# Performance work log

Measured on AMD Instinct MI355X. Metric: run time of the kernel, lower is better.

The kernel has to match this reference:

```python
import jax, jax.numpy as jnp
import numpy as np

B, HRES, WRES, C, HEADS, WS, SS = 32, 64, 64, 256, 8, 8, 4
N = WS * WS
HID = 4 * C
EPS = 1e-5


def _rel_pos_index(ws):
    coords = np.stack(np.meshgrid(np.arange(ws), np.arange(ws), indexing='ij'))  # [2,ws,ws]
    cf = coords.reshape(2, -1)
    rel = (cf[:, :, None] - cf[:, None, :]).transpose(1, 2, 0)  # [N,N,2]
    rel[:, :, 0] += ws - 1
    rel[:, :, 1] += ws - 1
    rel[:, :, 0] *= 2 * ws - 1
    return rel.sum(-1).reshape(-1)  # [N*N]


def _attn_mask(H, W, ws, ss):
    img = np.zeros((H, W))
    cnt = 0
    for hs in (slice(0, -ws), slice(-ws, -ss), slice(-ss, None)):
        for wsl in (slice(0, -ws), slice(-ws, -ss), slice(-ss, None)):
            img[hs, wsl] = cnt
            cnt += 1
    mw = img.reshape(H // ws, ws, W // ws, ws).transpose(0, 2, 1, 3).reshape(-1, ws * ws)
    am = mw[:, None, :] - mw[:, :, None]  # [nW,N,N]
    return np.where(am != 0, -100.0, 0.0).astype(np.float32)


_RPI = jnp.asarray(_rel_pos_index(WS))
_MASK = jnp.asarray(_attn_mask(HRES, WRES, WS, SS))  # [nW,N,N]


def _ln(x, g, b):
    m = x.mean(-1, keepdims=True)
    v = ((x - m) ** 2).mean(-1, keepdims=True)
    return (x - m) / jnp.sqrt(v + EPS) * g + b


def setup_inputs() -> dict:
    key = jax.random.key(0)
    ks = jax.random.split(key, 16)
    s = 0.02
    return {
        'x': jax.random.normal(ks[0], (B, HRES * WRES, C), jnp.float32),
        'norm1_g': jnp.ones((C,), jnp.float32),
        'norm1_b': jnp.zeros((C,), jnp.float32),
        'qkv_w': jax.random.normal(ks[1], (3 * C, C), jnp.float32) * s,
        'qkv_b': jnp.zeros((3 * C,), jnp.float32),
        'rpb_table': jax.random.normal(ks[2], ((2 * WS - 1) ** 2, HEADS), jnp.float32) * s,
        'proj_w': jax.random.normal(ks[3], (C, C), jnp.float32) * s,
        'proj_b': jnp.zeros((C,), jnp.float32),
        'norm2_g': jnp.ones((C,), jnp.float32),
        'norm2_b': jnp.zeros((C,), jnp.float32),
        'fc1_w': jax.random.normal(ks[4], (HID, C), jnp.float32) * s,
        'fc1_b': jnp.zeros((HID,), jnp.float32),
        'fc2_w': jax.random.normal(ks[5], (C, HID), jnp.float32) * s,
        'fc2_b': jnp.zeros((C,), jnp.float32),
        'H': HRES,
        'W': WRES,
    }


def reference(x, norm1_g, norm1_b, qkv_w, qkv_b, rpb_table, proj_w, proj_b,
              norm2_g, norm2_b, fc1_w, fc1_b, fc2_w, fc2_b, H, W):
    Bn, L, Cd = x.shape
    ws, ss, nh = WS, SS, HEADS
    hd = Cd // nh
    shortcut = x
    h = _ln(x, norm1_g, norm1_b).reshape(Bn, H, W, Cd)
    # cyclic shift (H,W divisible by ws -> no padding needed)
    h = jnp.roll(h, (-ss, -ss), axis=(1, 2))
    # window partition: [B,H,W,C] -> [B*nW, N, C]
    h = h.reshape(Bn, H // ws, ws, W // ws, ws, Cd).transpose(0, 1, 3, 2, 4, 5).reshape(-1, N, Cd)
    qkv = (h @ qkv_w.T + qkv_b).reshape(-1, N, 3, nh, hd).transpose(2, 0, 3, 1, 4)
    q, k, v = qkv[0], qkv[1], qkv[2]  # [B_,h,N,d]
    attn = jnp.einsum('bhnd,bhmd->bhnm', q * (hd ** -0.5), k)
    rpb = rpb_table[_RPI].reshape(N, N, nh).transpose(2, 0, 1)  # [h,N,N]
    attn = attn + rpb[None]
    nW = _MASK.shape[0]
    attn = attn.reshape(Bn, nW, nh, N, N) + _MASK[None, :, None]
    attn = jax.nn.softmax(attn.reshape(-1, nh, N, N), axis=-1)
    o = jnp.einsum('bhnm,bhmd->bhnd', attn, v).transpose(0, 2, 1, 3).reshape(-1, N, Cd)
    o = o @ proj_w.T + proj_b
    # window reverse + reverse shift
    o = o.reshape(Bn, H // ws, W // ws, ws, ws, Cd).transpose(0, 1, 3, 2, 4, 5).reshape(Bn, H, W, Cd)
    o = jnp.roll(o, (ss, ss), axis=(1, 2)).reshape(Bn, L, Cd)
    x = shortcut + o
    h2 = _ln(x, norm2_g, norm2_b)
    h2 = jax.nn.gelu(h2 @ fc1_w.T + fc1_b, approximate=False)
    return x + (h2 @ fc2_w.T + fc2_b)
```

## Files before the change

### kernel.cpp

```cpp
#include <hip/hip_runtime.h>
#include <hip/hip_bf16.h>
#include <stdint.h>

typedef __bf16 bf16_t;
typedef __bf16 bf16x8 __attribute__((ext_vector_type(8)));
typedef __bf16 bf16x4 __attribute__((ext_vector_type(4)));
typedef float f32x4 __attribute__((ext_vector_type(4)));

#define MROWS 131072

__device__ __forceinline__ bf16_t to_bf16(float f) {
  __hip_bfloat16 h = __float2bfloat16(f);
  return *reinterpret_cast<bf16_t*>(&h);
}

__device__ __forceinline__ f32x4 mfma16(bf16x8 a, bf16x8 b, f32x4 c) {
  return __builtin_amdgcn_mfma_f32_16x16x32_bf16(a, b, c, 0, 0, 0);
}

__device__ __forceinline__ void gload16(const void* g, void* l) {
  __builtin_amdgcn_global_load_lds(
      (const __attribute__((address_space(1))) void*)g,
      (__attribute__((address_space(3))) void*)l, 16, 0, 0);
}

__device__ __forceinline__ int map_row(int m) {
  int b   = m >> 12;
  int rem = m & 4095;
  int win = rem >> 6;
  int n   = rem & 63;
  int gh  = ((win >> 3) << 3) + (n >> 3);
  int gw  = ((win & 7) << 3) + (n & 7);
  int sh  = (gh + 4) & 63;
  int sw  = (gw + 4) & 63;
  return (b << 12) + (sh << 6) + sw;
}

__global__ __launch_bounds__(256) void cvt_all(const float* __restrict__ qkv_w,
                                               const float* __restrict__ proj_w,
                                               const float* __restrict__ fc1_w,
                                               const float* __restrict__ fc2_w,
                                               bf16_t* __restrict__ qkv_o,
                                               bf16_t* __restrict__ proj_o,
                                               bf16_t* __restrict__ fc1_o,
                                               bf16_t* __restrict__ fc2_o) {
  int i = blockIdx.x * 256 + threadIdx.x;
  if (i < 196608)       qkv_o[i] = to_bf16(qkv_w[i]);
  else if (i < 262144)  proj_o[i - 196608] = to_bf16(proj_w[i - 196608]);
  else if (i < 524288)  fc1_o[i - 262144] = to_bf16(fc1_w[i - 262144]);
  else                  fc2_o[i - 524288] = to_bf16(fc2_w[i - 524288]);
}

__global__ __launch_bounds__(256) void bias_kernel(const float* __restrict__ rpbt,
                                                   float* __restrict__ bias) {
  int idx = blockIdx.x * 256 + threadIdx.x;
  int m = idx & 63, n = (idx >> 6) & 63, h = (idx >> 12) & 7, c = idx >> 15;
  int yn = n >> 3, xn = n & 7, ym = m >> 3, xm = m & 7;
  float v = rpbt[((yn - ym + 7) * 15 + (xn - xm + 7)) * 8 + h];
  int rn = (c & 2) ? (yn < 4 ? 1 : 2) : 0;
  int cn = (c & 1) ? (xn < 4 ? 1 : 2) : 0;
  int rm = (c & 2) ? (ym < 4 ? 1 : 2) : 0;
  int cm = (c & 1) ? (xm < 4 ? 1 : 2) : 0;
  if (rn * 3 + cn != rm * 3 + cm) v -= 100.0f;
  bias[idx] = v;
}

template <bool PERM>
__global__ __launch_bounds__(256) void ln_kernel(const float* __restrict__ xin,
                                                 const float* __restrict__ g,
                                                 const float* __restrict__ b,
                                                 bf16_t* __restrict__ out) {
  int row  = (blockIdx.x << 2) + (threadIdx.x >> 6);
  int lane = threadIdx.x & 63;
  int src  = PERM ? map_row(row) : row;
  float4 v = *reinterpret_cast<const float4*>(xin + (size_t)src * 256 + (lane << 2));
  float s = v.x + v.y + v.z + v.w;
#pragma unroll
  for (int d = 1; d < 64; d <<= 1) s += __shfl_xor(s, d);
  float mean = s * 0.00390625f;
  float ax = v.x - mean, ay = v.y - mean, az = v.z - mean, aw = v.w - mean;
  float s2 = ax * ax + ay * ay + az * az + aw * aw;
#pragma unroll
  for (int d = 1; d < 64; d <<= 1) s2 += __shfl_xor(s2, d);
  float rstd = rsqrtf(s2 * 0.00390625f + 1e-5f);
  float4 gv = *reinterpret_cast<const float4*>(g + (lane << 2));
  float4 bv = *reinterpret_cast<const float4*>(b + (lane << 2));
  bf16x4 o4;
  o4[0] = to_bf16(ax * rstd * gv.x + bv.x);
  o4[1] = to_bf16(ay * rstd * gv.y + bv.y);
  o4[2] = to_bf16(az * rstd * gv.z + bv.z);
  o4[3] = to_bf16(aw * rstd * gv.w + bv.w);
  *reinterpret_cast<bf16x4*>(out + (size_t)row * 256 + (lane << 2)) = o4;
}

template <int EPI>
__global__ __launch_bounds__(1024) void gemm256p(const bf16_t* __restrict__ A,
                                                 const bf16_t* __restrict__ W,
                                                 const float* __restrict__ bias,
                                                 void* __restrict__ outp,
                                                 void* __restrict__ outp2,
                                                 void* __restrict__ outp3,
                                                 const float* __restrict__ resid,
                                                 const float* __restrict__ n2g,
                                                 const float* __restrict__ n2b,
                                                 bf16_t* __restrict__ x2n,
                                                 int M, int N, int K, int NBN) {
  extern __shared__ __align__(16) char smem[];
  bf16_t* As  = (bf16_t*)smem;
  bf16_t* Bs  = As + 32768;
  float*  lnS = (float*)(Bs + 32768);
  float*  lnQ = lnS + 1024;
  float*  lnMR = lnQ + 1024;
  const int tid  = threadIdx.x;
  const int lane = tid & 63, lo = lane & 15, hi = lane >> 4;
  const int wid  = tid >> 6, wm = wid >> 2, wn = wid & 3;
  const int cpx = gridDim.x >> 3;
  const int wg  = (blockIdx.x & 7) * cpx + (blockIdx.x >> 3);
  const int bn = (wg % NBN) << 8, bm = (wg / NBN) << 8;
  f32x4 acc[4][4] = {};

#define STG(buf, kt)                                                        \
  {                                                                         \
    _Pragma("unroll") for (int l = 0; l < 2; ++l) {                         \
      int ch = (l << 10) + tid;                                             \
      int row = ch >> 3, sl = (ch & 7) ^ (row & 7);                         \
      gload16(A + (size_t)(bm + row) * K + ((kt) << 6) + (sl << 3),         \
              &As[((buf) << 14) + (ch << 3)]);                              \
      gload16(W + (size_t)(bn + row) * K + ((kt) << 6) + (sl << 3),         \
              &Bs[((buf) << 14) + (ch << 3)]);                              \
    }                                                                       \
  }

  const int nt = K >> 6;
  STG(0, 0);
  STG(1, 1);
  asm volatile("s_waitcnt vmcnt(4)" ::: "memory");
  __builtin_amdgcn_s_barrier();

  const int arow = (wm << 6) + lo;
  const int brow = (wn << 6) + lo;
  for (int t = 0; t < nt; ++t) {
    const int p = t & 1;
    const bf16_t* as = &As[p << 14];
    const bf16_t* bs = &Bs[p << 14];
    bf16x8 af0[4], bf0[4];
#pragma unroll
    for (int mf = 0; mf < 4; ++mf) {
      int r = arow + (mf << 4);
      af0[mf] = *reinterpret_cast<const bf16x8*>(&as[(r << 6) + ((hi ^ (r & 7)) << 3)]);
    }
#pragma unroll
    for (int nf = 0; nf < 4; ++nf) {
      int r = brow + (nf << 4);
      bf0[nf] = *reinterpret_cast<const bf16x8*>(&bs[(r << 6) + ((hi ^ (r & 7)) << 3)]);
    }
    __builtin_amdgcn_s_setprio(1);
#pragma unroll
    for (int mf = 0; mf < 4; ++mf)
#pragma unroll
      for (int nf = 0; nf < 4; ++nf)
        acc[mf][nf] = mfma16(af0[mf], bf0[nf], acc[mf][nf]);
    __builtin_amdgcn_s_setprio(0);
    bf16x8 af1[4], bf1[4];
#pragma unroll
    for (int mf = 0; mf < 4; ++mf) {
      int r = arow + (mf << 4);
      af1[mf] = *reinterpret_cast<const bf16x8*>(&as[(r << 6) + (((4 + hi) ^ (r & 7)) << 3)]);
    }
#pragma unroll
    for (int nf = 0; nf < 4; ++nf) {
      int r = brow + (nf << 4);
      bf1[nf] = *reinterpret_cast<const bf16x8*>(&bs[(r << 6) + (((4 + hi) ^ (r & 7)) << 3)]);
    }
    asm volatile("s_waitcnt lgkmcnt(0)" ::: "memory");
    __builtin_amdgcn_sched_barrier(0);
    __builtin_amdgcn_s_barrier();
    if (t + 2 < nt) STG(p, t + 2);
    __builtin_amdgcn_s_setprio(1);
#pragma unroll
    for (int mf = 0; mf < 4; ++mf)
#pragma unroll
      for (int nf = 0; nf < 4; ++nf)
        acc[mf][nf] = mfma16(af1[mf], bf1[nf], acc[mf][nf]);
    __builtin_amdgcn_s_setprio(0);
    if (t + 2 < nt)      { asm volatile("s_waitcnt vmcnt(4)" ::: "memory"); }
    else if (t + 1 < nt) { asm volatile("s_waitcnt vmcnt(0)" ::: "memory"); }
    __builtin_amdgcn_s_barrier();
  }
#undef STG

  float bv4[4];
#pragma unroll
  for (int nf = 0; nf < 4; ++nf) bv4[nf] = bias[bn + (wn << 6) + (nf << 4) + lo];

  if constexpr (EPI == 2) {
    float* o = (float*)outp;
    float gv[4], bnv[4];
#pragma unroll
    for (int nf = 0; nf < 4; ++nf) {
      int col = bn + (wn << 6) + (nf << 4) + lo;
      gv[nf] = n2g[col]; bnv[nf] = n2b[col];
    }
#pragma unroll
    for (int mf = 0; mf < 4; ++mf)
#pragma unroll
      for (int r = 0; r < 4; ++r) {
        int rl = (wm << 6) + (mf << 4) + (hi << 2) + r;
        int xr = map_row(bm + rl);
        float s = 0.f, q = 0.f;
#pragma unroll
        for (int nf = 0; nf < 4; ++nf) {
          int col = bn + (wn << 6) + (nf << 4) + lo;
          size_t idx = (size_t)xr * 256 + col;
          float v = resid[idx] + acc[mf][nf][r] + bv4[nf];
          acc[mf][nf][r] = v;
          o[idx] = v;
          s += v; q += v * v;
        }
#pragma unroll
        for (int d = 1; d < 16; d <<= 1) { s += __shfl_xor(s, d); q += __shfl_xor(q, d); }
        if (lo == 0) { lnS[(rl << 2) + wn] = s; lnQ[(rl << 2) + wn] = q; }
      }
    __syncthreads();
    if (tid < 256) {
      float s = lnS[tid << 2] + lnS[(tid << 2) + 1] + lnS[(tid << 2) + 2] + lnS[(tid << 2) + 3];
      float q = lnQ[tid << 2] + lnQ[(tid << 2) + 1] + lnQ[(tid << 2) + 2] + lnQ[(tid << 2) + 3];
      float mean = s * 0.00390625f;
      float var  = q * 0.00390625f - mean * mean;
      lnMR[tid << 1] = mean;
      lnMR[(tid << 1) + 1] = rsqrtf(var + 1e-5f);
    }
    __syncthreads();
#pragma unroll
    for (int mf = 0; mf < 4; ++mf)
#pragma unroll
      for (int r = 0; r < 4; ++r) {
        int rl = (wm << 6) + (mf << 4) + (hi << 2) + r;
        int xr = map_row(bm + rl);
        float mean = lnMR[rl << 1], rstd = lnMR[(rl << 1) + 1];
#pragma unroll
        for (int nf = 0; nf < 4; ++nf) {
          int col = bn + (wn << 6) + (nf << 4) + lo;
          x2n[(size_t)xr * 256 + col] = to_bf16((acc[mf][nf][r] - mean) * rstd * gv[nf] + bnv[nf]);
        }
      }
  } else {
#pragma unroll
    for (int mf = 0; mf < 4; ++mf)
#pragma unroll
      for (int r = 0; r < 4; ++r) {
        int row = bm + (wm << 6) + (mf << 4) + (hi << 2) + r;
        if constexpr (EPI == 3) {
          float* o = (float*)outp;
#pragma unroll
          for (int nf = 0; nf < 4; ++nf) {
            int col = bn + (wn << 6) + (nf << 4) + lo;
            size_t idx = (size_t)row * 256 + col;
            o[idx] = o[idx] + acc[mf][nf][r] + bv4[nf];
          }
        } else if constexpr (EPI == 4) {
#pragma unroll
          for (int nf = 0; nf < 4; ++nf) {
            int col = bn + (wn << 6) + (nf << 4) + lo;
            bf16_t* base = (col < 256) ? (bf16_t*)outp
                          : (col < 512) ? (bf16_t*)outp2 : (bf16_t*)outp3;
            int hd = (col >> 5) & 7, d = col & 31;
            base[((size_t)hd * MROWS + row) * 32 + d] = to_bf16(acc[mf][nf][r] + bv4[nf]);
          }
        } else {
          bf16_t* o = (bf16_t*)outp;
#pragma unroll
          for (int nf = 0; nf < 4; ++nf) {
            int col = bn + (wn << 6) + (nf << 4) + lo;
            float v = acc[mf][nf][r] + bv4[nf];
            if constexpr (EPI == 1) v = 0.5f * v * (1.0f + erff(v * 0.70710678118654752f));
            o[(size_t)row * N + col] = to_bf16(v);
          }
        }
      }
  }
}

template <int EPI>
__global__ __launch_bounds__(256) void gemm_bt(const bf16_t* __restrict__ A,
                                               const bf16_t* __restrict__ W,
                                               const float* __restrict__ bias,
                                               void* __restrict__ outp,
                                               int M, int N, int K, int NBN) {
  __shared__ __align__(16) bf16_t As[3 * 128 * 32];
  __shared__ __align__(16) bf16_t Bs[3 * 128 * 32];
  const int tid  = threadIdx.x;
  const int lane = tid & 63, lo = lane & 15, hi = lane >> 4;
  const int wave = tid >> 6;
  const int cpx = gridDim.x >> 3;
  const int wg  = (blockIdx.x & 7) * cpx + (blockIdx.x >> 3);
  const int bn = (wg % NBN) << 7, bm = (wg / NBN) << 7;
  const int wr = (wave >> 1) << 6, wc = (wave & 1) << 6;
  f32x4 acc[4][4] = {};

#define STAGE(buf, kt)                                                         \
  {                                                                            \
    int k0s = (kt) << 5;                                                       \
    _Pragma("unroll") for (int it = 0; it < 2; ++it) {                         \
      int ch = (it << 8) + tid;                                                \
      int r = ch >> 2;                                                         \
      int kf = ((ch & 3) ^ ((r >> 1) & 3)) << 3;                               \
      gload16(A + (size_t)(bm + r) * K + k0s + kf, &As[((buf) << 12) + (ch << 3)]); \
      gload16(W + (size_t)(bn + r) * K + k0s + kf, &Bs[((buf) << 12) + (ch << 3)]); \
    }                                                                          \
  }

  const int nt = K >> 5;
  STAGE(0, 0);
  STAGE(1, 1);

  int cb = 0;
  for (int t = 0; t < nt; ++t) {
    if (t + 1 < nt) { asm volatile("s_waitcnt vmcnt(4)" ::: "memory"); }
    else            { asm volatile("s_waitcnt vmcnt(0)" ::: "memory"); }
    __builtin_amdgcn_s_barrier();
    if (t + 2 < nt) {
      int sb = (cb == 0) ? 2 : cb - 1;
      STAGE(sb, t + 2);
    }
    const bf16_t* as = &As[cb << 12];
    const bf16_t* bs = &Bs[cb << 12];
    bf16x8 af[4], bfr[4];
#pragma unroll
    for (int i = 0; i < 4; ++i) {
      int ra = wr + (i << 4) + lo;
      af[i] = *reinterpret_cast<const bf16x8*>(&as[ra * 32 + ((hi ^ ((ra >> 1) & 3)) << 3)]);
    }
#pragma unroll
    for (int j = 0; j < 4; ++j) {
      int rb = wc + (j << 4) + lo;
      bfr[j] = *reinterpret_cast<const bf16x8*>(&bs[rb * 32 + ((hi ^ ((rb >> 1) & 3)) << 3)]);
    }
    __builtin_amdgcn_s_setprio(1);
#pragma unroll
    for (int i = 0; i < 4; ++i)
#pragma unroll
      for (int j = 0; j < 4; ++j)
        acc[i][j] = mfma16(af[i], bfr[j], acc[i][j]);
    __builtin_amdgcn_s_setprio(0);
    cb = (cb == 2) ? 0 : cb + 1;
  }
#undef STAGE

  float bv[4];
#pragma unroll
  for (int j = 0; j < 4; ++j) bv[j] = bias[bn + wc + (j << 4) + lo];

#pragma unroll
  for (int i = 0; i < 4; ++i)
#pragma unroll
    for (int r = 0; r < 4; ++r) {
      int row = bm + wr + (i << 4) + (hi << 2) + r;
      float* o = (float*)outp;
#pragma unroll
      for (int j = 0; j < 4; ++j) {
        int col = bn + wc + (j << 4) + lo;
        size_t idx = (size_t)row * 256 + col;
        o[idx] = o[idx] + acc[i][j][r] + bv[j];
      }
    }
}

__global__ __launch_bounds__(256) void attn_kernel(const bf16_t* __restrict__ qh,
                                                   const bf16_t* __restrict__ kh,
                                                   const bf16_t* __restrict__ vh,
                                                   const float* __restrict__ bias,
                                                   bf16_t* __restrict__ o) {
  __shared__ __align__(16) bf16_t Pl[4][64 * 72];
  __shared__ __align__(16) bf16_t Vt[4][32 * 72];
  const int wave = threadIdx.x >> 6, lane = threadIdx.x & 63;
  const int lo = lane & 15, hi = lane >> 4;
  const int id = (blockIdx.x << 2) + wave;
  const int win = id >> 3, h = id & 7;
  const size_t hb = ((size_t)h * MROWS + (size_t)win * 64) * 32;
  const bf16_t* qb = qh + hb;
  const bf16_t* kb = kh + hb;
  const bf16_t* vb = vh + hb;

  const bf16_t* vbl = vb + lane * 32;
#pragma unroll
  for (int c4 = 0; c4 < 4; ++c4) {
    bf16x8 v8 = *reinterpret_cast<const bf16x8*>(vbl + (c4 << 3));
#pragma unroll
    for (int e = 0; e < 8; ++e) Vt[wave][((c4 << 3) + e) * 72 + lane] = v8[e];
  }

  bf16x8 qa[4], ka[4];
#pragma unroll
  for (int i = 0; i < 4; ++i)
    qa[i] = *reinterpret_cast<const bf16x8*>(qb + ((i << 4) + lo) * 32 + (hi << 3));
#pragma unroll
  for (int j = 0; j < 4; ++j)
    ka[j] = *reinterpret_cast<const bf16x8*>(kb + ((j << 4) + lo) * 32 + (hi << 3));
  f32x4 s[4][4] = {};
#pragma unroll
  for (int i = 0; i < 4; ++i)
#pragma unroll
    for (int j = 0; j < 4; ++j) s[i][j] = mfma16(qa[i], ka[j], s[i][j]);

  const int wh = (win & 63) >> 3, ww = win & 7;
  const int cls = ((wh == 7) ? 2 : 0) + ((ww == 7) ? 1 : 0);
  const float* bb = bias + ((size_t)cls * 8 + h) * 4096;
  const float scale = 0.17677669529663687f;

  float pinv[4][4];
#pragma unroll
  for (int i = 0; i < 4; ++i) {
#pragma unroll
    for (int r = 0; r < 4; ++r) {
      int n = (i << 4) + (hi << 2) + r;
      const float* brow = bb + n * 64 + lo;
      float vals[4], mx = -1e30f;
#pragma unroll
      for (int j = 0; j < 4; ++j) {
        float val = s[i][j][r] * scale + brow[j << 4];
        vals[j] = val;
        mx = fmaxf(mx, val);
      }
#pragma unroll
      for (int d = 1; d < 16; d <<= 1) mx = fmaxf(mx, __shfl_xor(mx, d));
      float sum = 0.0f;
#pragma unroll
      for (int j = 0; j < 4; ++j) {
        float p = __expf(vals[j] - mx);
        sum += p;
        Pl[wave][n * 72 + (j << 4) + lo] = to_bf16(p);
      }
#pragma unroll
      for (int d = 1; d < 16; d <<= 1) sum += __shfl_xor(sum, d);
      pinv[i][r] = 1.0f / sum;
    }
  }

  __syncthreads();

  f32x4 oa[4][2] = {};
#pragma unroll
  for (int kt = 0; kt < 2; ++kt) {
    bf16x8 pa[4], va[2];
#pragma unroll
    for (int i = 0; i < 4; ++i)
      pa[i] = *reinterpret_cast<const bf16x8*>(&Pl[wave][((i << 4) + lo) * 72 + (kt << 5) + (hi << 3)]);
#pragma unroll
    for (int dt = 0; dt < 2; ++dt)
      va[dt] = *reinterpret_cast<const bf16x8*>(&Vt[wave][((dt << 4) + lo) * 72 + (kt << 5) + (hi << 3)]);
#pragma unroll
    for (int i = 0; i < 4; ++i)
#pragma unroll
      for (int dt = 0; dt < 2; ++dt) oa[i][dt] = mfma16(pa[i], va[dt], oa[i][dt]);
  }

  bf16_t* ob = o + (size_t)win * (64 * 256) + h * 32;
#pragma unroll
  for (int i = 0; i < 4; ++i)
#pragma unroll
    for (int r = 0; r < 4; ++r) {
      int n = (i << 4) + (hi << 2) + r;
      float piv = pinv[i][r];
#pragma unroll
      for (int dt = 0; dt < 2; ++dt)
        ob[(size_t)n * 256 + (dt << 4) + lo] = to_bf16(oa[i][dt][r] * piv);
    }
}

extern "C" void kernel_launch(void* const* d_in, const int* in_sizes, int n_in,
                              void* d_out, int out_size, void* d_ws, size_t ws_size,
                              hipStream_t stream) {
  const float* x      = (const float*)d_in[0];
  const float* n1g    = (const float*)d_in[1];
  const float* n1b    = (const float*)d_in[2];
  const float* qkv_w  = (const float*)d_in[3];
  const float* qkv_b  = (const float*)d_in[4];
  const float* rpbt   = (const float*)d_in[5];
  const float* proj_w = (const float*)d_in[6];
  const float* proj_b = (const float*)d_in[7];
  const float* n2g    = (const float*)d_in[8];
  const float* n2b    = (const float*)d_in[9];
  const float* fc1_w  = (const float*)d_in[10];
  const float* fc1_b  = (const float*)d_in[11];
  const float* fc2_w  = (const float*)d_in[12];
  const float* fc2_b  = (const float*)d_in[13];
  float* out = (float*)d_out;
  char*  ws  = (char*)d_ws;

  const size_t MB64 = 67108864;
  bf16_t* hln  = (bf16_t*)(ws);
  bf16_t* obuf = (bf16_t*)(ws);
  bf16_t* h2   = (bf16_t*)(ws);
  bf16_t* qbuf = (bf16_t*)(ws + MB64);
  bf16_t* x2n  = (bf16_t*)(ws + MB64);
  bf16_t* wb   = (bf16_t*)(ws + 2 * MB64);
  bf16_t* qkv_wb  = wb;
  bf16_t* proj_wb = qkv_wb + 196608;
  bf16_t* fc1_wb  = proj_wb + 65536;
  bf16_t* fc2_wb  = fc1_wb + 262144;
  float*  biast   = (float*)(fc2_wb + 262144);
  bf16_t* kbuf = (bf16_t*)d_out;
  bf16_t* vbuf = kbuf + 33554432;

  const int SMEM_G = 131072;
  const int SMEM_P = 141312;
  hipFuncSetAttribute(reinterpret_cast<const void*>(gemm256p<1>),
                      hipFuncAttributeMaxDynamicSharedMemorySize, SMEM_G);
  hipFuncSetAttribute(reinterpret_cast<const void*>(gemm256p<2>),
                      hipFuncAttributeMaxDynamicSharedMemorySize, SMEM_P);
  hipFuncSetAttribute(reinterpret_cast<const void*>(gemm256p<4>),
                      hipFuncAttributeMaxDynamicSharedMemorySize, SMEM_G);

  cvt_all<<<3072, 256, 0, stream>>>(qkv_w, proj_w, fc1_w, fc2_w,
                                    qkv_wb, proj_wb, fc1_wb, fc2_wb);
  bias_kernel<<<512, 256, 0, stream>>>(rpbt, biast);

  ln_kernel<true><<<32768, 256, 0, stream>>>(x, n1g, n1b, hln);

  gemm256p<4><<<1536, 1024, SMEM_G, stream>>>(hln, qkv_wb, qkv_b, qbuf, kbuf, vbuf,
                                              nullptr, nullptr, nullptr, nullptr,
                                              MROWS, 768, 256, 3);

  attn_kernel<<<4096, 256, 0, stream>>>(qbuf, kbuf, vbuf, biast, obuf);

  gemm256p<2><<<512, 1024, SMEM_P, stream>>>(obuf, proj_wb, proj_b, out, nullptr, nullptr,
                                             x, n2g, n2b, x2n, MROWS, 256, 256, 1);

  for (int c = 0; c < 4; ++c) {
    const bf16_t* xa = x2n + (size_t)c * 32768 * 256;
    gemm256p<1><<<512, 1024, SMEM_G, stream>>>(xa, fc1_wb, fc1_b, h2, nullptr, nullptr,
                                               nullptr, nullptr, nullptr, nullptr,
                                               32768, 1024, 256, 4);
    gemm_bt<3><<<512, 256, 0, stream>>>(h2, fc2_wb, fc2_b, out + (size_t)c * 32768 * 256,
                                        32768, 256, 1024, 2);
  }
}
```

Measured before the change: 612.1 us.

## Replace 256x256 GEMM with 128x256 tile, BK=32, triple-buffered LDS pipeline

Rewrites the main GEMM kernel to use 128x256 output tiles with 512 threads and a K-step of 32, storing three LDS stages instead of two 256x256 stages. The smaller shared-memory footprint and launch bounds of (512,4) are meant to let several blocks share a CU, so latency hiding comes from occupancy and a deeper prefetch. The epilogues are simplified on the assumption that each block covers exactly one 256-column slab, and the unused EPI==3 path is dropped. The cost is a smaller tile, so each loaded weight element is reused less, and there are more barriers per unit of K.

```diff
diff --git a/kernel.cpp b/kernel.cpp
--- a/kernel.cpp
+++ b/kernel.cpp
@@ -94,98 +94,82 @@
 }
 
 template <int EPI>
-__global__ __launch_bounds__(1024) void gemm256p(const bf16_t* __restrict__ A,
-                                                 const bf16_t* __restrict__ W,
-                                                 const float* __restrict__ bias,
-                                                 void* __restrict__ outp,
-                                                 void* __restrict__ outp2,
-                                                 void* __restrict__ outp3,
-                                                 const float* __restrict__ resid,
-                                                 const float* __restrict__ n2g,
-                                                 const float* __restrict__ n2b,
-                                                 bf16_t* __restrict__ x2n,
-                                                 int M, int N, int K, int NBN) {
+__global__ __launch_bounds__(512, 4) void gemm128x256(const bf16_t* __restrict__ A,
+                                                      const bf16_t* __restrict__ W,
+                                                      const float* __restrict__ bias,
+                                                      void* __restrict__ outp,
+                                                      void* __restrict__ outp2,
+                                                      void* __restrict__ outp3,
+                                                      const float* __restrict__ resid,
+                                                      const float* __restrict__ n2g,
+                                                      const float* __restrict__ n2b,
+                                                      bf16_t* __restrict__ x2n,
+                                                      int M, int N, int K, int NBN) {
   extern __shared__ __align__(16) char smem[];
   bf16_t* As  = (bf16_t*)smem;
-  bf16_t* Bs  = As + 32768;
-  float*  lnS = (float*)(Bs + 32768);
-  float*  lnQ = lnS + 1024;
-  float*  lnMR = lnQ + 1024;
+  bf16_t* Bs  = As + 3 * 4096;
+  float*  lnS = (float*)(Bs + 3 * 8192);
+  float*  lnQ = lnS + 512;
+  float*  lnMR = lnQ + 512;
   const int tid  = threadIdx.x;
   const int lane = tid & 63, lo = lane & 15, hi = lane >> 4;
   const int wid  = tid >> 6, wm = wid >> 2, wn = wid & 3;
   const int cpx = gridDim.x >> 3;
   const int wg  = (blockIdx.x & 7) * cpx + (blockIdx.x >> 3);
-  const int bn = (wg % NBN) << 8, bm = (wg / NBN) << 8;
+  const int bn = (wg % NBN) << 8, bm = (wg / NBN) << 7;
   f32x4 acc[4][4] = {};
 
-#define STG(buf, kt)                                                        \
-  {                                                                         \
-    _Pragma("unroll") for (int l = 0; l < 2; ++l) {                         \
-      int ch = (l << 10) + tid;                                             \
-      int row = ch >> 3, sl = (ch & 7) ^ (row & 7);                         \
-      gload16(A + (size_t)(bm + row) * K + ((kt) << 6) + (sl << 3),         \
-              &As[((buf) << 14) + (ch << 3)]);                              \
-      gload16(W + (size_t)(bn + row) * K + ((kt) << 6) + (sl << 3),         \
-              &Bs[((buf) << 14) + (ch << 3)]);                              \
-    }                                                                       \
-  }
-
-  const int nt = K >> 6;
+#define STG(buf, kt)                                                          \
+  {                                                                           \
+    int k0s = (kt) << 5;                                                      \
+    {                                                                         \
+      int ch = tid;                                                           \
+      int row = ch >> 2, sl = ((ch & 3) ^ ((row >> 1) & 3)) << 3;             \
+      gload16(A + (size_t)(bm + row) * K + k0s + sl,                          \
+              &As[((buf) << 12) + (ch << 3)]);                                \
+    }                                                                         \
+    _Pragma("unroll") for (int l = 0; l < 2; ++l) {                           \
+      int ch = (l << 9) + tid;                                                \
+      int row = ch >> 2, sl = ((ch & 3) ^ ((row >> 1) & 3)) << 3;             \
+      gload16(W + (size_t)(bn + row) * K + k0s + sl,                          \
+              &Bs[((buf) << 13) + (ch << 3)]);                                \
+    }                                                                         \
+  }
+
+  const int nt = K >> 5;
   STG(0, 0);
   STG(1, 1);
-  asm volatile("s_waitcnt vmcnt(4)" ::: "memory");
-  __builtin_amdgcn_s_barrier();
-
-  const int arow = (wm << 6) + lo;
-  const int brow = (wn << 6) + lo;
+
+  int cb = 0;
   for (int t = 0; t < nt; ++t) {
-    const int p = t & 1;
-    const bf16_t* as = &As[p << 14];
-    const bf16_t* bs = &Bs[p << 14];
-    bf16x8 af0[4], bf0[4];
-#pragma unroll
-    for (int mf = 0; mf < 4; ++mf) {
-      int r = arow + (mf << 4);
-      af0[mf] = *reinterpret_cast<const bf16x8*>(&as[(r << 6) + ((hi ^ (r & 7)) << 3)]);
-    }
-#pragma unroll
-    for (int nf = 0; nf < 4; ++nf) {
-      int r = brow + (nf << 4);
-      bf0[nf] = *reinterpret_cast<const bf16x8*>(&bs[(r << 6) + ((hi ^ (r & 7)) << 3)]);
+    if (t + 1 < nt) { asm volatile("s_waitcnt vmcnt(3)" ::: "memory"); }
+    else            { asm volatile("s_waitcnt vmcnt(0)" ::: "memory"); }
+    __builtin_amdgcn_s_barrier();
+    if (t + 2 < nt) {
+      int sb = (cb == 0) ? 2 : cb - 1;
+      STG(sb, t + 2);
+    }
+    const bf16_t* as = &As[cb << 12];
+    const bf16_t* bs = &Bs[cb << 13];
+    bf16x8 af[4], bfr[4];
+#pragma unroll
+    for (int i = 0; i < 4; ++i) {
+      int ra = (wm << 6) + (i << 4) + lo;
+      af[i] = *reinterpret_cast<const bf16x8*>(&as[ra * 32 + ((hi ^ ((ra >> 1) & 3)) << 3)]);
+    }
+#pragma unroll
+    for (int j = 0; j < 4; ++j) {
+      int rb = (wn << 6) + (j << 4) + lo;
+      bfr[j] = *reinterpret_cast<const bf16x8*>(&bs[rb * 32 + ((hi ^ ((rb >> 1) & 3)) << 3)]);
     }
     __builtin_amdgcn_s_setprio(1);
 #pragma unroll
-    for (int mf = 0; mf < 4; ++mf)
-#pragma unroll
-      for (int nf = 0; nf < 4; ++nf)
-        acc[mf][nf] = mfma16(af0[mf], bf0[nf], acc[mf][nf]);
+    for (int i = 0; i < 4; ++i)
+#pragma unroll
+      for (int j = 0; j < 4; ++j)
+        acc[i][j] = mfma16(af[i], bfr[j], acc[i][j]);
     __builtin_amdgcn_s_setprio(0);
-    bf16x8 af1[4], bf1[4];
-#pragma unroll
-    for (int mf = 0; mf < 4; ++mf) {
-      int r = arow + (mf << 4);
-      af1[mf] = *reinterpret_cast<const bf16x8*>(&as[(r << 6) + (((4 + hi) ^ (r & 7)) << 3)]);
-    }
-#pragma unroll
-    for (int nf = 0; nf < 4; ++nf) {
-      int r = brow + (nf << 4);
-      bf1[nf] = *reinterpret_cast<const bf16x8*>(&bs[(r << 6) + (((4 + hi) ^ (r & 7)) << 3)]);
-    }
-    asm volatile("s_waitcnt lgkmcnt(0)" ::: "memory");
-    __builtin_amdgcn_sched_barrier(0);
-    __builtin_amdgcn_s_barrier();
-    if (t + 2 < nt) STG(p, t + 2);
-    __builtin_amdgcn_s_setprio(1);
-#pragma unroll
-    for (int mf = 0; mf < 4; ++mf)
-#pragma unroll
-      for (int nf = 0; nf < 4; ++nf)
-        acc[mf][nf] = mfma16(af1[mf], bf1[nf], acc[mf][nf]);
-    __builtin_amdgcn_s_setprio(0);
-    if (t + 2 < nt)      { asm volatile("s_waitcnt vmcnt(4)" ::: "memory"); }
-    else if (t + 1 < nt) { asm volatile("s_waitcnt vmcnt(0)" ::: "memory"); }
-    __builtin_amdgcn_s_barrier();
+    cb = (cb == 2) ? 0 : cb + 1;
   }
 #undef STG
 
@@ -198,7 +182,7 @@
     float gv[4], bnv[4];
 #pragma unroll
     for (int nf = 0; nf < 4; ++nf) {
-      int col = bn + (wn << 6) + (nf << 4) + lo;
+      int col = (wn << 6) + (nf << 4) + lo;
       gv[nf] = n2g[col]; bnv[nf] = n2b[col];
     }
 #pragma unroll
@@ -210,7 +194,7 @@
         float s = 0.f, q = 0.f;
 #pragma unroll
         for (int nf = 0; nf < 4; ++nf) {
-          int col = bn + (wn << 6) + (nf << 4) + lo;
+          int col = (wn << 6) + (nf << 4) + lo;
           size_t idx = (size_t)xr * 256 + col;
           float v = resid[idx] + acc[mf][nf][r] + bv4[nf];
           acc[mf][nf][r] = v;
@@ -222,7 +206,7 @@
         if (lo == 0) { lnS[(rl << 2) + wn] = s; lnQ[(rl << 2) + wn] = q; }
       }
     __syncthreads();
-    if (tid < 256) {
+    if (tid < 128) {
       float s = lnS[tid << 2] + lnS[(tid << 2) + 1] + lnS[(tid << 2) + 2] + lnS[(tid << 2) + 3];
       float q = lnQ[tid << 2] + lnQ[(tid << 2) + 1] + lnQ[(tid << 2) + 2] + lnQ[(tid << 2) + 3];
       float mean = s * 0.00390625f;
@@ -240,7 +224,7 @@
         float mean = lnMR[rl << 1], rstd = lnMR[(rl << 1) + 1];
 #pragma unroll
         for (int nf = 0; nf < 4; ++nf) {
-          int col = bn + (wn << 6) + (nf << 4) + lo;
+          int col = (wn << 6) + (nf << 4) + lo;
           x2n[(size_t)xr * 256 + col] = to_bf16((acc[mf][nf][r] - mean) * rstd * gv[nf] + bnv[nf]);
         }
       }
@@ -250,21 +234,13 @@
 #pragma unroll
       for (int r = 0; r < 4; ++r) {
         int row = bm + (wm << 6) + (mf << 4) + (hi << 2) + r;
-        if constexpr (EPI == 3) {
-          float* o = (float*)outp;
+        if constexpr (EPI == 4) {
+          bf16_t* base = (bn == 0) ? (bf16_t*)outp
+                        : (bn == 256) ? (bf16_t*)outp2 : (bf16_t*)outp3;
 #pragma unroll
           for (int nf = 0; nf < 4; ++nf) {
-            int col = bn + (wn << 6) + (nf << 4) + lo;
-            size_t idx = (size_t)row * 256 + col;
-            o[idx] = o[idx] + acc[mf][nf][r] + bv4[nf];
-          }
-        } else if constexpr (EPI == 4) {
-#pragma unroll
-          for (int nf = 0; nf < 4; ++nf) {
-            int col = bn + (wn << 6) + (nf << 4) + lo;
-            bf16_t* base = (col < 256) ? (bf16_t*)outp
-                          : (col < 512) ? (bf16_t*)outp2 : (bf16_t*)outp3;
-            int hd = (col >> 5) & 7, d = col & 31;
+            int col = (wn << 6) + (nf << 4) + lo;
+            int hd = col >> 5, d = col & 31;
             base[((size_t)hd * MROWS + row) * 32 + d] = to_bf16(acc[mf][nf][r] + bv4[nf]);
           }
         } else {
@@ -503,13 +479,13 @@
   bf16_t* kbuf = (bf16_t*)d_out;
   bf16_t* vbuf = kbuf + 33554432;
 
-  const int SMEM_G = 131072;
-  const int SMEM_P = 141312;
-  hipFuncSetAttribute(reinterpret_cast<const void*>(gemm256p<1>),
+  const int SMEM_G = 73728;
+  const int SMEM_P = 78848;
+  hipFuncSetAttribute(reinterpret_cast<const void*>(gemm128x256<1>),
                       hipFuncAttributeMaxDynamicSharedMemorySize, SMEM_G);
-  hipFuncSetAttribute(reinterpret_cast<const void*>(gemm256p<2>),
+  hipFuncSetAttribute(reinterpret_cast<const void*>(gemm128x256<2>),
                       hipFuncAttributeMaxDynamicSharedMemorySize, SMEM_P);
-  hipFuncSetAttribute(reinterpret_cast<const void*>(gemm256p<4>),
+  hipFuncSetAttribute(reinterpret_cast<const void*>(gemm128x256<4>),
                       hipFuncAttributeMaxDynamicSharedMemorySize, SMEM_G);
 
   cvt_all<<<3072, 256, 0, stream>>>(qkv_w, proj_w, fc1_w, fc2_w,
@@ -518,20 +494,20 @@
 
   ln_kernel<true><<<32768, 256, 0, stream>>>(x, n1g, n1b, hln);
 
-  gemm256p<4><<<1536, 1024, SMEM_G, stream>>>(hln, qkv_wb, qkv_b, qbuf, kbuf, vbuf,
-                                              nullptr, nullptr, nullptr, nullptr,
-                                              MROWS, 768, 256, 3);
+  gemm128x256<4><<<3072, 512, SMEM_G, stream>>>(hln, qkv_wb, qkv_b, qbuf, kbuf, vbuf,
+                                                nullptr, nullptr, nullptr, nullptr,
+                                                MROWS, 768, 256, 3);
 
   attn_kernel<<<4096, 256, 0, stream>>>(qbuf, kbuf, vbuf, biast, obuf);
 
-  gemm256p<2><<<512, 1024, SMEM_P, stream>>>(obuf, proj_wb, proj_b, out, nullptr, nullptr,
-                                             x, n2g, n2b, x2n, MROWS, 256, 256, 1);
+  gemm128x256<2><<<1024, 512, SMEM_P, stream>>>(obuf, proj_wb, proj_b, out, nullptr, nullptr,
+                                                x, n2g, n2b, x2n, MROWS, 256, 256, 1);
 
   for (int c = 0; c < 4; ++c) {
     const bf16_t* xa = x2n + (size_t)c * 32768 * 256;
-    gemm256p<1><<<512, 1024, SMEM_G, stream>>>(xa, fc1_wb, fc1_b, h2, nullptr, nullptr,
-                                               nullptr, nullptr, nullptr, nullptr,
-                                               32768, 1024, 256, 4);
+    gemm128x256<1><<<1024, 512, SMEM_G, stream>>>(xa, fc1_wb, fc1_b, h2, nullptr, nullptr,
+                                                  nullptr, nullptr, nullptr, nullptr,
+                                                  32768, 1024, 256, 4);
     gemm_bt<3><<<512, 256, 0, stream>>>(h2, fc2_wb, fc2_b, out + (size_t)c * 32768 * 256,
                                         32768, 256, 1024, 2);
   }
```

Result: faster. 599.3 us (-2.1%).
